# Kernel optimization log

Hardware: AMD Instinct MI355X
Metric: run time of the kernel (lower is better)

Reference implementation:

```python
import jax, jax.numpy as jnp
import numpy as np

DELTA_V = 0.5
DELTA_D = 1.5
ALPHA = 1.0
BETA = 1.0
GAMMA = 0.001
K = 64  # max number of instance ids per batch element


def _safe_sqrt(sq):
    # sqrt with zero-safe gradient: exact where sq > 0, returns 0 otherwise
    pos = sq > 0
    return jnp.sqrt(jnp.where(pos, sq, 1.0)) * pos.astype(sq.dtype)


def setup_inputs() -> dict:
    key = jax.random.key(0)
    k1, k2 = jax.random.split(key)
    B, N, D = 16, 65536, 32
    embeddings = jax.random.normal(k1, (B, N, D), dtype=jnp.float32)
    instance_ids = jax.random.randint(k2, (B, N), 0, K, dtype=jnp.int32)
    mask = jnp.ones((B, N), dtype=bool)
    return {"embeddings": embeddings, "instance_ids": instance_ids, "mask": mask}


def reference(embeddings, instance_ids, mask):
    B, N, D = embeddings.shape
    f32 = embeddings.dtype
    valid = mask & (instance_ids >= 0)
    # flat segment id per point; invalid points go to dump segment B*K
    batch_off = jnp.arange(B, dtype=jnp.int32)[:, None] * K
    seg = jnp.where(valid, batch_off + instance_ids, B * K).reshape(-1)
    w = valid.reshape(-1).astype(f32)
    flat = embeddings.reshape(-1, D)

    # per-instance sums / counts -> means  (segment reduce, memory-bound)
    sums = jax.ops.segment_sum(flat * w[:, None], seg, num_segments=B * K + 1)[: B * K]
    counts = jax.ops.segment_sum(w, seg, num_segments=B * K + 1)[: B * K]
    means_flat = sums / jnp.maximum(counts, 1.0)[:, None]  # (B*K, D)
    present = (counts > 0).reshape(B, K)                   # (B, K)
    num_inst = present.sum(-1).astype(f32)                 # (B,)
    valid_b = (num_inst >= 2).astype(f32)                  # batches counted as samples

    # ---- variance (pull) loss ----
    seg_clip = jnp.minimum(seg, B * K - 1)
    diff = flat - means_flat[seg_clip]                     # (B*N, D)
    dist = _safe_sqrt((diff * diff).sum(-1))
    pen = jnp.maximum(dist - DELTA_V, 0.0) ** 2 * w
    inst_pen = jax.ops.segment_sum(pen, seg, num_segments=B * K + 1)[: B * K]
    inst_pen = (inst_pen / jnp.maximum(counts, 1.0)).reshape(B, K)
    var_b = (inst_pen * present).sum(-1) / jnp.maximum(num_inst, 1.0)

    # ---- distance (push) loss: pairwise over instance means ----
    means = means_flat.reshape(B, K, D)
    dsq = ((means[:, :, None, :] - means[:, None, :, :]) ** 2).sum(-1)  # (B, K, K)
    iu = jnp.arange(K)
    pair_m = present[:, :, None] & present[:, None, :] & (iu[:, None] < iu[None, :])
    pair_mf = pair_m.astype(f32)
    pdist = _safe_sqrt(jnp.where(pair_m, dsq, 1.0)) * pair_mf
    pen2 = jnp.maximum(2.0 * DELTA_D - pdist, 0.0) ** 2 * pair_mf
    num_pairs = num_inst * (num_inst - 1.0) / 2.0
    dist_b = pen2.sum((1, 2)) / jnp.maximum(num_pairs, 1.0)

    # ---- regularization loss ----
    mnorm = _safe_sqrt((means * means).sum(-1)) * present.astype(f32)  # (B, K)
    reg_b = mnorm.sum(-1) / jnp.maximum(num_inst, 1.0)

    denom = jnp.maximum(valid_b.sum(), 1.0)
    var_loss = (var_b * valid_b).sum() / denom
    dist_loss = (dist_b * valid_b).sum() / denom
    reg_loss = (reg_b * valid_b).sum() / denom
    total = ALPHA * var_loss + BETA * dist_loss + GAMMA * reg_loss
    return jnp.stack([total, var_loss, dist_loss, reg_loss])
```

## Files before the change

kernel.cpp:

```cpp
#include <hip/hip_runtime.h>
#include <cstdint>

#define BB 16
#define NN 65536
#define DD 32
#define KK 64
#define DELTA_V 0.5f
#define DELTA_D 1.5f

typedef short bf16x8 __attribute__((ext_vector_type(8)));
typedef float f32x16 __attribute__((ext_vector_type(16)));

__device__ __forceinline__ short f2bf(float x) {
    union { float f; unsigned u; } v; v.f = x;
    const unsigned r = v.u + 0x7FFFu + ((v.u >> 16) & 1u);
    return (short)(r >> 16);
}

#define K1_BPB 64
#define K1_PPB 1024
#define K1_WPTS 256

__global__ __launch_bounds__(256, 4) void k_accum(
    const float* __restrict__ emb, const int* __restrict__ ids,
    const int* __restrict__ mask, float* __restrict__ parts,
    float* __restrict__ pcnt)
{
    __shared__ float tb[4][64][33];
    __shared__ float lc2[4][KK];
    const int tid  = threadIdx.x;
    const int w    = tid >> 6, lane = tid & 63;
    const int half = lane >> 5, d32 = lane & 31;
    const int b    = blockIdx.x >> 6;
    const int blk  = blockIdx.x & 63;
    const size_t pw = (size_t)b * NN + (size_t)blk * K1_PPB + (size_t)w * K1_WPTS;

    f32x16 acc0 = {}, acc1 = {};
    int c0 = 0, c1 = 0;
    const int m0 = d32, m1 = d32 + 32;
    float (*T)[33] = tb[w];

    for (int s = 0; s < 4; ++s) {
        const size_t ps = pw + s * 64;
        const float4* ep = (const float4*)(emb + (ps + lane) * DD);
        float4 r[8];
#pragma unroll
        for (int q = 0; q < 8; ++q) r[q] = ep[q];
        const int idr = ids[ps + lane];
        const int mkr = mask[ps + lane];
        const int vid = (mkr != 0 && (unsigned)idr < KK) ? idr : -1;

        float* myrow = T[lane];
#pragma unroll
        for (int q = 0; q < 8; ++q) {
            myrow[4 * q + 0] = r[q].x; myrow[4 * q + 1] = r[q].y;
            myrow[4 * q + 2] = r[q].z; myrow[4 * q + 3] = r[q].w;
        }

#pragma unroll
        for (int q = 0; q < 4; ++q) {
            bf16x8 bfB, a0, a1;
#pragma unroll
            for (int e = 0; e < 8; ++e) {
                bfB[e] = f2bf(T[q * 16 + 8 * half + e][d32]);
                const int s_lo = __builtin_amdgcn_readlane(vid, q * 16 + e);
                const int s_hi = __builtin_amdgcn_readlane(vid, q * 16 + 8 + e);
                const int sel  = half ? s_hi : s_lo;
                const bool h0 = (sel == m0), h1 = (sel == m1);
                a0[e] = h0 ? (short)0x3F80 : (short)0;
                a1[e] = h1 ? (short)0x3F80 : (short)0;
                c0 += h0 ? 1 : 0;
                c1 += h1 ? 1 : 0;
            }
            acc0 = __builtin_amdgcn_mfma_f32_32x32x16_bf16(a0, bfB, acc0, 0, 0, 0);
            acc1 = __builtin_amdgcn_mfma_f32_32x32x16_bf16(a1, bfB, acc1, 0, 0, 0);
        }
    }
    __syncthreads();

#pragma unroll
    for (int r = 0; r < 16; ++r) {
        const int mrow = (r & 3) + 8 * (r >> 2) + 4 * half;
        T[mrow][d32]      = acc0[r];
        T[32 + mrow][d32] = acc1[r];
    }
    c0 += __shfl_down(c0, 32);
    c1 += __shfl_down(c1, 32);
    if (lane < 32) { lc2[w][lane] = (float)c0; lc2[w][lane + 32] = (float)c1; }
    __syncthreads();

    float* pb = parts + (size_t)blockIdx.x * (KK * DD);
    for (int i = tid; i < KK * DD; i += 256) {
        const int row = i >> 5, col = i & 31;
        pb[i] = tb[0][row][col] + tb[1][row][col] + tb[2][row][col] + tb[3][row][col];
    }
    if (tid < KK)
        pcnt[(size_t)blockIdx.x * KK + tid] =
            lc2[0][tid] + lc2[1][tid] + lc2[2][tid] + lc2[3][tid];
}

__global__ __launch_bounds__(256) void k_reduce_push(
    const float* __restrict__ parts, const float* __restrict__ pcnt,
    float* __restrict__ mu, float* __restrict__ regb,
    float* __restrict__ distb)
{
    const int b = blockIdx.x;
    const int tid = threadIdx.x;
    __shared__ float lm[KK][DD + 1];
    __shared__ float lcnt[KK];
    __shared__ float red[4];

    if (tid < KK) {
        float s = 0.f;
        for (int j = 0; j < K1_BPB; ++j)
            s += pcnt[((size_t)b * K1_BPB + j) * KK + tid];
        lcnt[tid] = s;
        mu[(size_t)b * KK * 33 + tid * 33 + 32] = s;
    }
    __syncthreads();

    for (int e = tid; e < KK * DD; e += 256) {
        float s = 0.f;
        for (int j = 0; j < K1_BPB; ++j)
            s += parts[((size_t)b * K1_BPB + j) * (KK * DD) + e];
        const int k = e >> 5, d = e & 31;
        const float m = s / fmaxf(lcnt[k], 1.f);
        lm[k][d] = m;
        mu[(size_t)b * KK * 33 + k * 33 + d] = m;
    }
    __syncthreads();

    float ninst = 0.f;
    if (tid < KK) {
        const float c = lcnt[tid];
        const float pres = (c > 0.f) ? 1.f : 0.f;
        float sq = 0.f;
#pragma unroll
        for (int d = 0; d < DD; ++d) { const float m = lm[tid][d]; sq = fmaf(m, m, sq); }
        float nm = ((sq > 0.f) ? sqrtf(sq) : 0.f) * pres;
        float pn = pres;
        for (int off = 32; off; off >>= 1) {
            pn += __shfl_down(pn, off);
            nm += __shfl_down(nm, off);
        }
        if (tid == 0) {
            ninst = pn;
            regb[b] = nm / fmaxf(pn, 1.f);
        }
    }

    float acc = 0.f;
    for (int idx = tid; idx < KK * KK; idx += 256) {
        const int i = idx >> 6, j = idx & 63;
        if (i < j && lcnt[i] > 0.f && lcnt[j] > 0.f) {
            float dsq = 0.f;
#pragma unroll
            for (int d = 0; d < DD; ++d) {
                const float df = lm[i][d] - lm[j][d];
                dsq = fmaf(df, df, dsq);
            }
            const float pd = (dsq > 0.f) ? sqrtf(dsq) : 0.f;
            const float pen = fmaxf(2.f * DELTA_D - pd, 0.f);
            acc = fmaf(pen, pen, acc);
        }
    }
    for (int off = 32; off; off >>= 1) acc += __shfl_down(acc, off);
    if ((tid & 63) == 0) red[tid >> 6] = acc;
    __syncthreads();
    if (tid == 0) {
        const float tot = red[0] + red[1] + red[2] + red[3];
        const float np = ninst * (ninst - 1.f) * 0.5f;
        distb[b] = tot / fmaxf(np, 1.f);
    }
}

#define K2_BPB 64
#define K2_PTS (NN / K2_BPB)

__global__ __launch_bounds__(256) void k_pull(
    const float* __restrict__ emb, const int* __restrict__ ids,
    const int* __restrict__ mask, const float* __restrict__ mu,
    float* __restrict__ varpart)
{
    __shared__ float smu[KK * 33];
    __shared__ float red[4];
    const int tid = threadIdx.x;
    const int b   = blockIdx.x >> 6;
    const int blk = blockIdx.x & 63;

    const float* mub = mu + (size_t)b * KK * 33;
    for (int i = tid; i < KK * 33; i += 256) smu[i] = mub[i];
    __syncthreads();

    const size_t p0 = (size_t)b * NN + (size_t)blk * K2_PTS;
    float accv = 0.f;
    for (int p = tid; p < K2_PTS; p += 256) {
        const int id = ids[p0 + p];
        const bool v = (mask[p0 + p] != 0) && ((unsigned)id < KK);
        const int sid = v ? id : 0;
        const float* mr = smu + sid * 33;
        const float4* e = (const float4*)(emb + (p0 + p) * DD);
        float dsq = 0.f;
#pragma unroll
        for (int q = 0; q < 8; ++q) {
            const float4 t = e[q];
            float a;
            a = t.x - mr[4 * q + 0]; dsq = fmaf(a, a, dsq);
            a = t.y - mr[4 * q + 1]; dsq = fmaf(a, a, dsq);
            a = t.z - mr[4 * q + 2]; dsq = fmaf(a, a, dsq);
            a = t.w - mr[4 * q + 3]; dsq = fmaf(a, a, dsq);
        }
        const float dist = (dsq > 0.f) ? sqrtf(dsq) : 0.f;
        float pen = fmaxf(dist - DELTA_V, 0.f);
        pen = pen * pen;
        if (v) accv += pen / fmaxf(mr[32], 1.f);
    }
    for (int off = 32; off; off >>= 1) accv += __shfl_down(accv, off);
    if ((tid & 63) == 0) red[tid >> 6] = accv;
    __syncthreads();
    if (tid == 0)
        varpart[blockIdx.x] = red[0] + red[1] + red[2] + red[3];
}

__global__ __launch_bounds__(64) void k_final(
    const float* __restrict__ mu, const float* __restrict__ varpart,
    const float* __restrict__ regb, const float* __restrict__ distb,
    float* __restrict__ out)
{
    const int tid = threadIdx.x;
    __shared__ float s_var[BB], s_valid[BB];
    if (tid < BB) {
        const int b = tid;
        float ni = 0.f;
        for (int k = 0; k < KK; ++k)
            ni += (mu[(size_t)b * KK * 33 + k * 33 + 32] > 0.f) ? 1.f : 0.f;
        float vs = 0.f;
        for (int j = 0; j < K2_BPB; ++j) vs += varpart[b * K2_BPB + j];
        s_var[tid]   = vs / fmaxf(ni, 1.f);
        s_valid[tid] = (ni >= 2.f) ? 1.f : 0.f;
    }
    __syncthreads();
    if (tid == 0) {
        float denom = 0.f, v = 0.f, d = 0.f, r = 0.f;
        for (int b = 0; b < BB; ++b) {
            const float vb = s_valid[b];
            denom += vb;
            v += s_var[b] * vb;
            d += distb[b] * vb;
            r += regb[b] * vb;
        }
        denom = fmaxf(denom, 1.f);
        v /= denom; d /= denom; r /= denom;
        out[0] = v + d + 0.001f * r;
        out[1] = v;
        out[2] = d;
        out[3] = r;
    }
}

extern "C" void kernel_launch(void* const* d_in, const int* in_sizes, int n_in,
                              void* d_out, int out_size, void* d_ws, size_t ws_size,
                              hipStream_t stream)
{
    const float* emb  = (const float*)d_in[0];
    const int*   ids  = (const int*)d_in[1];
    const int*   mask = (const int*)d_in[2];

    float* ws      = (float*)d_ws;
    float* parts   = ws;
    float* pcnt    = parts + (size_t)BB * K1_BPB * KK * DD;
    float* mu      = pcnt + (size_t)BB * K1_BPB * KK;
    float* varpart = mu + (size_t)BB * KK * 33;
    float* regb    = varpart + BB * K2_BPB;
    float* distb   = regb + BB;

    k_accum<<<BB * K1_BPB, 256, 0, stream>>>(emb, ids, mask, parts, pcnt);
    k_reduce_push<<<BB, 256, 0, stream>>>(parts, pcnt, mu, regb, distb);
    k_pull<<<BB * K2_BPB, 256, 0, stream>>>(emb, ids, mask, mu, varpart);
    k_final<<<1, 64, 0, stream>>>(mu, varpart, regb, distb, (float*)d_out);
}
```

Before: 100.9 us.

## Coalesce embedding loads in accum and pull kernels with 8-lane-per-point layout

Both streaming kernels now load embeddings so consecutive lanes read consecutive float4s: eight lanes cover one point, and the per-lane stride across point rows is gone. In k_accum the tile is written to LDS as float4 rows with a 36-float pitch, and a block-wide barrier is dropped. In k_pull, eight lanes cooperate on one point, reduce the squared distance with xor shuffles, and multiply by a precomputed reciprocal count stored in a padded 36-wide mean table. The aim is to fix uncoalesced global reads on the memory-bound passes, at the cost of extra shuffles and some idle lanes in the per-point epilogue.

```diff
diff --git a/kernel.cpp b/kernel.cpp
--- a/kernel.cpp
+++ b/kernel.cpp
@@ -19,43 +19,41 @@
 
 #define K1_BPB 64
 #define K1_PPB 1024
-#define K1_WPTS 256
 
 __global__ __launch_bounds__(256, 4) void k_accum(
     const float* __restrict__ emb, const int* __restrict__ ids,
     const int* __restrict__ mask, float* __restrict__ parts,
     float* __restrict__ pcnt)
 {
-    __shared__ float tb[4][64][33];
+    __shared__ float tb[4][64][36];
     __shared__ float lc2[4][KK];
     const int tid  = threadIdx.x;
     const int w    = tid >> 6, lane = tid & 63;
     const int half = lane >> 5, d32 = lane & 31;
+    const int pl   = lane >> 3;
+    const int pc   = lane & 7;
     const int b    = blockIdx.x >> 6;
     const int blk  = blockIdx.x & 63;
-    const size_t pw = (size_t)b * NN + (size_t)blk * K1_PPB + (size_t)w * K1_WPTS;
+    const size_t pw = (size_t)b * NN + (size_t)blk * K1_PPB + (size_t)w * 256;
 
     f32x16 acc0 = {}, acc1 = {};
     int c0 = 0, c1 = 0;
     const int m0 = d32, m1 = d32 + 32;
-    float (*T)[33] = tb[w];
+    float (*T)[36] = tb[w];
 
     for (int s = 0; s < 4; ++s) {
         const size_t ps = pw + s * 64;
-        const float4* ep = (const float4*)(emb + (ps + lane) * DD);
+        const float4* ep4 = (const float4*)(emb + ps * DD);
         float4 r[8];
 #pragma unroll
-        for (int q = 0; q < 8; ++q) r[q] = ep[q];
+        for (int i = 0; i < 8; ++i) r[i] = ep4[i * 64 + lane];
         const int idr = ids[ps + lane];
         const int mkr = mask[ps + lane];
         const int vid = (mkr != 0 && (unsigned)idr < KK) ? idr : -1;
 
-        float* myrow = T[lane];
-#pragma unroll
-        for (int q = 0; q < 8; ++q) {
-            myrow[4 * q + 0] = r[q].x; myrow[4 * q + 1] = r[q].y;
-            myrow[4 * q + 2] = r[q].z; myrow[4 * q + 3] = r[q].w;
-        }
+#pragma unroll
+        for (int i = 0; i < 8; ++i)
+            *(float4*)&T[i * 8 + pl][4 * pc] = r[i];
 
 #pragma unroll
         for (int q = 0; q < 4; ++q) {
@@ -76,7 +74,6 @@
             acc1 = __builtin_amdgcn_mfma_f32_32x32x16_bf16(a1, bfB, acc1, 0, 0, 0);
         }
     }
-    __syncthreads();
 
 #pragma unroll
     for (int r = 0; r < 16; ++r) {
@@ -115,7 +112,8 @@
         for (int j = 0; j < K1_BPB; ++j)
             s += pcnt[((size_t)b * K1_BPB + j) * KK + tid];
         lcnt[tid] = s;
-        mu[(size_t)b * KK * 33 + tid * 33 + 32] = s;
+        mu[(size_t)b * KK * 36 + tid * 36 + 32] = s;
+        mu[(size_t)b * KK * 36 + tid * 36 + 33] = 1.f / fmaxf(s, 1.f);
     }
     __syncthreads();
 
@@ -126,7 +124,7 @@
         const int k = e >> 5, d = e & 31;
         const float m = s / fmaxf(lcnt[k], 1.f);
         lm[k][d] = m;
-        mu[(size_t)b * KK * 33 + k * 33 + d] = m;
+        mu[(size_t)b * KK * 36 + k * 36 + d] = m;
     }
     __syncthreads();
 
@@ -175,48 +173,59 @@
 }
 
 #define K2_BPB 64
-#define K2_PTS (NN / K2_BPB)
+#define K2_PTS 1024
 
 __global__ __launch_bounds__(256) void k_pull(
     const float* __restrict__ emb, const int* __restrict__ ids,
     const int* __restrict__ mask, const float* __restrict__ mu,
     float* __restrict__ varpart)
 {
-    __shared__ float smu[KK * 33];
+    __shared__ float smu[KK][36];
     __shared__ float red[4];
     const int tid = threadIdx.x;
+    const int w = tid >> 6, lane = tid & 63;
+    const int pl = lane >> 3;
+    const int pc = lane & 7;
     const int b   = blockIdx.x >> 6;
     const int blk = blockIdx.x & 63;
 
-    const float* mub = mu + (size_t)b * KK * 33;
-    for (int i = tid; i < KK * 33; i += 256) smu[i] = mub[i];
-    __syncthreads();
-
-    const size_t p0 = (size_t)b * NN + (size_t)blk * K2_PTS;
+    const float* mub = mu + (size_t)b * KK * 36;
+    for (int i = tid; i < KK * 36; i += 256) ((float*)smu)[i] = mub[i];
+    __syncthreads();
+
+    const size_t p0 = (size_t)b * NN + (size_t)blk * K2_PTS + (size_t)w * 256;
     float accv = 0.f;
-    for (int p = tid; p < K2_PTS; p += 256) {
-        const int id = ids[p0 + p];
-        const bool v = (mask[p0 + p] != 0) && ((unsigned)id < KK);
-        const int sid = v ? id : 0;
-        const float* mr = smu + sid * 33;
-        const float4* e = (const float4*)(emb + (p0 + p) * DD);
-        float dsq = 0.f;
-#pragma unroll
-        for (int q = 0; q < 8; ++q) {
-            const float4 t = e[q];
-            float a;
-            a = t.x - mr[4 * q + 0]; dsq = fmaf(a, a, dsq);
-            a = t.y - mr[4 * q + 1]; dsq = fmaf(a, a, dsq);
-            a = t.z - mr[4 * q + 2]; dsq = fmaf(a, a, dsq);
-            a = t.w - mr[4 * q + 3]; dsq = fmaf(a, a, dsq);
-        }
-        const float dist = (dsq > 0.f) ? sqrtf(dsq) : 0.f;
-        float pen = fmaxf(dist - DELTA_V, 0.f);
-        pen = pen * pen;
-        if (v) accv += pen / fmaxf(mr[32], 1.f);
+    for (int t = 0; t < 4; ++t) {
+        const size_t pt0 = p0 + t * 64;
+        const int idr = ids[pt0 + lane];
+        const int mkr = mask[pt0 + lane];
+        const int vid = (mkr != 0 && (unsigned)idr < KK) ? idr : -1;
+        const float4* ep4 = (const float4*)(emb + pt0 * DD);
+#pragma unroll
+        for (int g = 0; g < 8; ++g) {
+            const float4 x = ep4[g * 64 + lane];
+            const int sid = __shfl(vid, g * 8 + pl);
+            const int row = (sid >= 0) ? sid : 0;
+            const float4 m4 = *(const float4*)&smu[row][4 * pc];
+            float dsq;
+            {
+                float a = x.x - m4.x; dsq = a * a;
+                a = x.y - m4.y; dsq = fmaf(a, a, dsq);
+                a = x.z - m4.z; dsq = fmaf(a, a, dsq);
+                a = x.w - m4.w; dsq = fmaf(a, a, dsq);
+            }
+            dsq += __shfl_xor(dsq, 1);
+            dsq += __shfl_xor(dsq, 2);
+            dsq += __shfl_xor(dsq, 4);
+            if (pc == 0 && sid >= 0) {
+                const float dist = (dsq > 0.f) ? sqrtf(dsq) : 0.f;
+                float pen = fmaxf(dist - DELTA_V, 0.f);
+                accv = fmaf(pen * pen, smu[row][33], accv);
+            }
+        }
     }
     for (int off = 32; off; off >>= 1) accv += __shfl_down(accv, off);
-    if ((tid & 63) == 0) red[tid >> 6] = accv;
+    if (lane == 0) red[w] = accv;
     __syncthreads();
     if (tid == 0)
         varpart[blockIdx.x] = red[0] + red[1] + red[2] + red[3];
@@ -233,7 +242,7 @@
         const int b = tid;
         float ni = 0.f;
         for (int k = 0; k < KK; ++k)
-            ni += (mu[(size_t)b * KK * 33 + k * 33 + 32] > 0.f) ? 1.f : 0.f;
+            ni += (mu[(size_t)b * KK * 36 + k * 36 + 32] > 0.f) ? 1.f : 0.f;
         float vs = 0.f;
         for (int j = 0; j < K2_BPB; ++j) vs += varpart[b * K2_BPB + j];
         s_var[tid]   = vs / fmaxf(ni, 1.f);
@@ -270,7 +279,7 @@
     float* parts   = ws;
     float* pcnt    = parts + (size_t)BB * K1_BPB * KK * DD;
     float* mu      = pcnt + (size_t)BB * K1_BPB * KK;
-    float* varpart = mu + (size_t)BB * KK * 33;
+    float* varpart = mu + (size_t)BB * KK * 36;
     float* regb    = varpart + BB * K2_BPB;
     float* distb   = regb + BB;
 
```

Result: faster. 96.03 us (-4.9%).
